# Kernel tuning notes

Hardware: AMD Instinct MI355X
Metric: run time of the kernel (lower is better)

The kernel has to match this reference:

```python
import jax, jax.numpy as jnp
import numpy as np

B, S, E, KD = 4, 2048, 1024, 1024

def setup_inputs() -> dict:
    key = jax.random.key(0)
    k1, k2, k3, k4 = jax.random.split(key, 4)
    # nn.Linear weights are [out_features, in_features]
    x = jax.random.normal(k1, (B, S, E), dtype=jnp.float32)
    W_q = jax.random.normal(k2, (KD, E), dtype=jnp.float32) * (E ** -0.5)
    W_k = jax.random.normal(k3, (KD, E), dtype=jnp.float32) * (E ** -0.5)
    W_v = jax.random.normal(k4, (E, E), dtype=jnp.float32) * (E ** -0.5)
    return {"x": x, "W_q": W_q, "W_k": W_k, "W_v": W_v}

def reference(x, W_q, W_k, W_v):
    # Projections: y = x @ W.T  (torch Linear convention)
    Q = jnp.einsum('bse,ke->bsk', x, W_q)   # [B,S,KD]
    K = jnp.einsum('bse,ke->bsk', x, W_k)   # [B,S,KD]
    V = jnp.einsum('bse,fe->bsf', x, W_v)   # [B,S,E]
    key_dim = W_q.shape[0]
    scores = jnp.einsum('bqk,bsk->bqs', Q, K) / jnp.sqrt(jnp.asarray(key_dim, x.dtype))
    S_len = x.shape[1]
    causal = jnp.tril(jnp.ones((S_len, S_len), dtype=bool))  # [S,S]
    scores = jnp.where(causal, scores, -jnp.inf)
    weights = jax.nn.softmax(scores, axis=-1)                # [B,S,S]
    out = jnp.einsum('bqs,bsf->bqf', weights, V)             # [B,S,E]
    return out
```

## Files before the change

kernel.cpp:

```cpp
#include <hip/hip_runtime.h>

typedef _Float16 f16;
typedef _Float16 f16x8 __attribute__((ext_vector_type(8)));
typedef float    f32x4 __attribute__((ext_vector_type(4)));

__device__ __forceinline__ void gld_lds16(const void* g, void* l) {
    __builtin_amdgcn_global_load_lds((__attribute__((address_space(1))) void*)g,
                                     (__attribute__((address_space(3))) void*)l,
                                     16, 0, 0);
}

template<typename OutT, int MODE>
__global__ void __launch_bounds__(256)
gemm_bt(const f16* __restrict__ A, const f16* __restrict__ B, OutT* __restrict__ C,
        int lda, int ldb, int ldc, int K, float scale,
        long sA, long sB, long sC)
{
    const int bz = blockIdx.z;
    A += (long)bz * sA;
    B += (long)bz * sB;
    C += (long)bz * sC;

    const int i0 = blockIdx.y * 128;
    const int j0 = blockIdx.x * 64;
    if (MODE == 1 && j0 >= i0 + 128) return;
    int Keff = K;
    if (MODE == 2) Keff = min(K, i0 + 128);

    __shared__ f16 As[128 * 64] __attribute__((aligned(16)));
    __shared__ f16 Bs[64 * 64]  __attribute__((aligned(16)));

    const int tid  = threadIdx.x;
    const int lane = tid & 63;
    const int wave = tid >> 6;
    const int row16 = lane & 15;
    const int quad  = lane >> 4;
    const int swz   = row16 & 7;
    const int wr = (wave >> 1) * 64;
    const int wc = (wave & 1) * 32;

    const int srow = tid >> 3;
    const int scol = ((tid & 7) ^ (srow & 7)) * 8;
    const f16* gA = A + (long)(i0 + srow) * lda + scol;
    const f16* gB = B + (long)(j0 + srow) * ldb + scol;
    f16* lA = As + tid * 8;
    f16* lB = Bs + tid * 8;

    f32x4 acc[4][2] = {};

    for (int k0 = 0; k0 < Keff; k0 += 64) {
        gld_lds16(gA + k0,                  lA);
        gld_lds16(gA + k0 + (long)32 * lda, lA + 32 * 64);
        gld_lds16(gA + k0 + (long)64 * lda, lA + 64 * 64);
        gld_lds16(gA + k0 + (long)96 * lda, lA + 96 * 64);
        gld_lds16(gB + k0,                  lB);
        gld_lds16(gB + k0 + (long)32 * ldb, lB + 32 * 64);
        __syncthreads();

        #pragma unroll
        for (int kk = 0; kk < 2; kk++) {
            f16x8 af[4], bf[2];
            #pragma unroll
            for (int t = 0; t < 4; t++)
                af[t] = *(const f16x8*)(As + (wr + t * 16 + row16) * 64
                                           + (((kk * 4 + quad) ^ swz) * 8));
            #pragma unroll
            for (int t = 0; t < 2; t++)
                bf[t] = *(const f16x8*)(Bs + (wc + t * 16 + row16) * 64
                                           + (((kk * 4 + quad) ^ swz) * 8));
            #pragma unroll
            for (int mt = 0; mt < 4; mt++)
                #pragma unroll
                for (int nt = 0; nt < 2; nt++)
                    acc[mt][nt] = __builtin_amdgcn_mfma_f32_16x16x32_f16(
                        af[mt], bf[nt], acc[mt][nt], 0, 0, 0);
        }
        __syncthreads();
    }

    #pragma unroll
    for (int mt = 0; mt < 4; mt++) {
        const int r0 = i0 + wr + mt * 16 + quad * 4;
        #pragma unroll
        for (int nt = 0; nt < 2; nt++) {
            const int c = j0 + wc + nt * 16 + row16;
            #pragma unroll
            for (int r = 0; r < 4; r++)
                C[(long)(r0 + r) * ldc + c] = (OutT)(acc[mt][nt][r] * scale);
        }
    }
}

__global__ void __launch_bounds__(256)
softmax_causal(f16* __restrict__ Sc)
{
    const int S = 2048;
    const long rowg = blockIdx.x;
    const long b = rowg >> 11;
    const int  i = (int)(rowg & 2047);
    f16* row = Sc + ((b * S + i) * (long)S);

    const int tid = threadIdx.x;
    const int c0  = tid * 8;
    const int lane = tid & 63, wave = tid >> 6;

    f16x8 in = *(const f16x8*)(row + c0);
    float v[8];
    float m = -3.4e38f;
    #pragma unroll
    for (int j = 0; j < 8; j++) {
        const bool ok = (c0 + j) <= i;
        v[j] = ok ? (float)in[j] : -3.4e38f;
        m = fmaxf(m, v[j]);
    }
    #pragma unroll
    for (int off = 32; off > 0; off >>= 1)
        m = fmaxf(m, __shfl_down(m, off, 64));
    __shared__ float redm[4];
    if (lane == 0) redm[wave] = m;
    __syncthreads();
    const float m0 = fmaxf(fmaxf(redm[0], redm[1]), fmaxf(redm[2], redm[3]));

    float e[8];
    float s = 0.f;
    #pragma unroll
    for (int j = 0; j < 8; j++) {
        const bool ok = (c0 + j) <= i;
        e[j] = ok ? __expf(v[j] - m0) : 0.f;
        s += e[j];
    }
    #pragma unroll
    for (int off = 32; off > 0; off >>= 1)
        s += __shfl_down(s, off, 64);
    __shared__ float reds[4];
    if (lane == 0) reds[wave] = s;
    __syncthreads();
    const float inv = 1.f / (reds[0] + reds[1] + reds[2] + reds[3]);

    f16x8 o;
    #pragma unroll
    for (int j = 0; j < 8; j++) o[j] = (f16)(e[j] * inv);
    *(f16x8*)(row + c0) = o;
}

__global__ void __launch_bounds__(256)
convert_all(const float* __restrict__ x, const float* __restrict__ Wq,
            const float* __restrict__ Wk, const float* __restrict__ Wv,
            f16* __restrict__ xh, f16* __restrict__ wh)
{
    const long blk = blockIdx.x;
    const float* src;
    f16* dst;
    long base;
    if (blk < 4096)      { src = x;  dst = xh;                    base = blk * 2048; }
    else if (blk < 4608) { src = Wq; dst = wh;                    base = (blk - 4096) * 2048; }
    else if (blk < 5120) { src = Wk; dst = wh + 1024L * 1024;     base = (blk - 4608) * 2048; }
    else                 { src = Wv; dst = wh + 2L * 1024 * 1024; base = (blk - 5120) * 2048; }
    const long i = base + (long)threadIdx.x * 8;
    f32x4 a = *(const f32x4*)(src + i);
    f32x4 b = *(const f32x4*)(src + i + 4);
    f16x8 o;
    o[0] = (f16)a[0]; o[1] = (f16)a[1]; o[2] = (f16)a[2]; o[3] = (f16)a[3];
    o[4] = (f16)b[0]; o[5] = (f16)b[1]; o[6] = (f16)b[2]; o[7] = (f16)b[3];
    *(f16x8*)(dst + i) = o;
}

extern "C" void kernel_launch(void* const* d_in, const int* in_sizes, int n_in,
                              void* d_out, int out_size, void* d_ws, size_t ws_size,
                              hipStream_t stream)
{
    (void)in_sizes; (void)n_in; (void)out_size; (void)ws_size;
    const float* x  = (const float*)d_in[0];
    const float* Wq = (const float*)d_in[1];
    const float* Wk = (const float*)d_in[2];
    const float* Wv = (const float*)d_in[3];
    float* out = (float*)d_out;

    const long NX = 4L * 2048 * 1024;
    const long NW = 1024L * 1024;

    char* p = (char*)d_ws;
    f16* xh  = (f16*)p; p += NX * 2;
    f16* wh  = (f16*)p; p += 3 * NW * 2;
    f16* QKh = (f16*)p; p += 2 * NX * 2;
    f16* Vt  = (f16*)p; p += NX * 2;
    f16* Sc  = (f16*)p; p += 4L * 2048 * 2048 * 2;
    f16* wvh = wh + 2L * NW;

    convert_all<<<5632, 256, 0, stream>>>(x, Wq, Wk, Wv, xh, wh);

    gemm_bt<f16, 0><<<dim3(32, 64, 1), 256, 0, stream>>>(
        xh, wh, QKh, 1024, 1024, 2048, 1024, 1.f, 0, 0, 0);
    gemm_bt<f16, 0><<<dim3(128, 8, 1), 256, 0, stream>>>(
        wvh, xh, Vt, 1024, 1024, 8192, 1024, 1.f, 0, 0, 0);

    gemm_bt<f16, 1><<<dim3(32, 16, 4), 256, 0, stream>>>(
        QKh, QKh + 1024, Sc, 2048, 2048, 2048, 1024, 0.03125f,
        2048L * 2048, 2048L * 2048, 2048L * 2048);

    softmax_causal<<<4 * 2048, 256, 0, stream>>>(Sc);

    gemm_bt<float, 2><<<dim3(16, 16, 4), 256, 0, stream>>>(
        Sc, Vt, out, 2048, 8192, 1024, 2048, 1.f,
        2048L * 2048, 2048L, 2048L * 1024);
}
```

Before: 250.1 us.

## Use 128x128 GEMM tiles, triangular block mapping, and skip masked softmax columns

```diff
diff --git a/kernel.cpp b/kernel.cpp
--- a/kernel.cpp
+++ b/kernel.cpp
@@ -21,14 +21,23 @@
     B += (long)bz * sB;
     C += (long)bz * sC;
 
-    const int i0 = blockIdx.y * 128;
-    const int j0 = blockIdx.x * 64;
-    if (MODE == 1 && j0 >= i0 + 128) return;
+    int bx = blockIdx.x, by = blockIdx.y;
+    if (MODE == 1) {
+        const int t = bx;
+        int y = 0;
+        while (((y + 1) * (y + 2)) >> 1 <= t) y++;
+        by = y;
+        bx = t - ((y * (y + 1)) >> 1);
+    }
+    if (MODE == 2 && (blockIdx.z & 2)) by = (int)gridDim.y - 1 - by;
+
+    const int i0 = by * 128;
+    const int j0 = bx * 128;
     int Keff = K;
     if (MODE == 2) Keff = min(K, i0 + 128);
 
     __shared__ f16 As[128 * 64] __attribute__((aligned(16)));
-    __shared__ f16 Bs[64 * 64]  __attribute__((aligned(16)));
+    __shared__ f16 Bs[128 * 64] __attribute__((aligned(16)));
 
     const int tid  = threadIdx.x;
     const int lane = tid & 63;
@@ -37,7 +46,7 @@
     const int quad  = lane >> 4;
     const int swz   = row16 & 7;
     const int wr = (wave >> 1) * 64;
-    const int wc = (wave & 1) * 32;
+    const int wc = (wave & 1) * 64;
 
     const int srow = tid >> 3;
     const int scol = ((tid & 7) ^ (srow & 7)) * 8;
@@ -46,32 +55,30 @@
     f16* lA = As + tid * 8;
     f16* lB = Bs + tid * 8;
 
-    f32x4 acc[4][2] = {};
+    f32x4 acc[4][4] = {};
 
     for (int k0 = 0; k0 < Keff; k0 += 64) {
-        gld_lds16(gA + k0,                  lA);
-        gld_lds16(gA + k0 + (long)32 * lda, lA + 32 * 64);
-        gld_lds16(gA + k0 + (long)64 * lda, lA + 64 * 64);
-        gld_lds16(gA + k0 + (long)96 * lda, lA + 96 * 64);
-        gld_lds16(gB + k0,                  lB);
-        gld_lds16(gB + k0 + (long)32 * ldb, lB + 32 * 64);
+        #pragma unroll
+        for (int p = 0; p < 4; p++) {
+            gld_lds16(gA + k0 + (long)(p * 32) * lda, lA + p * 32 * 64);
+            gld_lds16(gB + k0 + (long)(p * 32) * ldb, lB + p * 32 * 64);
+        }
         __syncthreads();
 
         #pragma unroll
         for (int kk = 0; kk < 2; kk++) {
-            f16x8 af[4], bf[2];
+            f16x8 af[4], bf[4];
             #pragma unroll
-            for (int t = 0; t < 4; t++)
+            for (int t = 0; t < 4; t++) {
                 af[t] = *(const f16x8*)(As + (wr + t * 16 + row16) * 64
                                            + (((kk * 4 + quad) ^ swz) * 8));
-            #pragma unroll
-            for (int t = 0; t < 2; t++)
                 bf[t] = *(const f16x8*)(Bs + (wc + t * 16 + row16) * 64
                                            + (((kk * 4 + quad) ^ swz) * 8));
+            }
             #pragma unroll
             for (int mt = 0; mt < 4; mt++)
                 #pragma unroll
-                for (int nt = 0; nt < 2; nt++)
+                for (int nt = 0; nt < 4; nt++)
                     acc[mt][nt] = __builtin_amdgcn_mfma_f32_16x16x32_f16(
                         af[mt], bf[nt], acc[mt][nt], 0, 0, 0);
         }
@@ -82,7 +89,7 @@
     for (int mt = 0; mt < 4; mt++) {
         const int r0 = i0 + wr + mt * 16 + quad * 4;
         #pragma unroll
-        for (int nt = 0; nt < 2; nt++) {
+        for (int nt = 0; nt < 4; nt++) {
             const int c = j0 + wc + nt * 16 + row16;
             #pragma unroll
             for (int r = 0; r < 4; r++)
@@ -99,19 +106,23 @@
     const long b = rowg >> 11;
     const int  i = (int)(rowg & 2047);
     f16* row = Sc + ((b * S + i) * (long)S);
+    const int L = ((i >> 7) + 1) << 7;
 
     const int tid = threadIdx.x;
     const int c0  = tid * 8;
     const int lane = tid & 63, wave = tid >> 6;
-
-    f16x8 in = *(const f16x8*)(row + c0);
+    const bool act = c0 < L;
+
     float v[8];
     float m = -3.4e38f;
-    #pragma unroll
-    for (int j = 0; j < 8; j++) {
-        const bool ok = (c0 + j) <= i;
-        v[j] = ok ? (float)in[j] : -3.4e38f;
-        m = fmaxf(m, v[j]);
+    if (act) {
+        f16x8 in = *(const f16x8*)(row + c0);
+        #pragma unroll
+        for (int j = 0; j < 8; j++) {
+            const bool ok = (c0 + j) <= i;
+            v[j] = ok ? (float)in[j] : -3.4e38f;
+            m = fmaxf(m, v[j]);
+        }
     }
     #pragma unroll
     for (int off = 32; off > 0; off >>= 1)
@@ -123,11 +134,13 @@
 
     float e[8];
     float s = 0.f;
-    #pragma unroll
-    for (int j = 0; j < 8; j++) {
-        const bool ok = (c0 + j) <= i;
-        e[j] = ok ? __expf(v[j] - m0) : 0.f;
-        s += e[j];
+    if (act) {
+        #pragma unroll
+        for (int j = 0; j < 8; j++) {
+            const bool ok = (c0 + j) <= i;
+            e[j] = ok ? __expf(v[j] - m0) : 0.f;
+            s += e[j];
+        }
     }
     #pragma unroll
     for (int off = 32; off > 0; off >>= 1)
@@ -137,10 +150,12 @@
     __syncthreads();
     const float inv = 1.f / (reds[0] + reds[1] + reds[2] + reds[3]);
 
-    f16x8 o;
-    #pragma unroll
-    for (int j = 0; j < 8; j++) o[j] = (f16)(e[j] * inv);
-    *(f16x8*)(row + c0) = o;
+    if (act) {
+        f16x8 o;
+        #pragma unroll
+        for (int j = 0; j < 8; j++) o[j] = (f16)(e[j] * inv);
+        *(f16x8*)(row + c0) = o;
+    }
 }
 
 __global__ void __launch_bounds__(256)
@@ -189,18 +204,18 @@
 
     convert_all<<<5632, 256, 0, stream>>>(x, Wq, Wk, Wv, xh, wh);
 
-    gemm_bt<f16, 0><<<dim3(32, 64, 1), 256, 0, stream>>>(
+    gemm_bt<f16, 0><<<dim3(16, 64, 1), 256, 0, stream>>>(
         xh, wh, QKh, 1024, 1024, 2048, 1024, 1.f, 0, 0, 0);
-    gemm_bt<f16, 0><<<dim3(128, 8, 1), 256, 0, stream>>>(
+    gemm_bt<f16, 0><<<dim3(64, 8, 1), 256, 0, stream>>>(
         wvh, xh, Vt, 1024, 1024, 8192, 1024, 1.f, 0, 0, 0);
 
-    gemm_bt<f16, 1><<<dim3(32, 16, 4), 256, 0, stream>>>(
+    gemm_bt<f16, 1><<<dim3(136, 1, 4), 256, 0, stream>>>(
         QKh, QKh + 1024, Sc, 2048, 2048, 2048, 1024, 0.03125f,
         2048L * 2048, 2048L * 2048, 2048L * 2048);
 
     softmax_causal<<<4 * 2048, 256, 0, stream>>>(Sc);
 
-    gemm_bt<float, 2><<<dim3(16, 16, 4), 256, 0, stream>>>(
+    gemm_bt<float, 2><<<dim3(8, 16, 4), 256, 0, stream>>>(
         Sc, Vt, out, 2048, 8192, 1024, 2048, 1.f,
         2048L * 2048, 2048L, 2048L * 1024);
 }
```

After: 255.8 us. +2.3%, slower.
